# Kernel optimization log

Measured on AMD Instinct MI355X. Metric: run time of the kernel, lower is better.

Reference implementation:

```python
import jax, jax.numpy as jnp
import numpy as np

HEADS = 8


def setup_inputs() -> dict:
    key = jax.random.key(0)
    k1, k2, k3, k4, k5 = jax.random.split(key, 5)
    bt, b_sz, n, dim = 2, 4, 1024, 512
    inner6 = 3072  # inner_dim * 6 where inner_dim = heads * dim_head = 512
    return {
        "x": jax.random.normal(k1, (bt, b_sz, n, dim), dtype=jnp.float32),
        "W_qkv": jax.random.normal(k2, (dim, inner6), dtype=jnp.float32) * 0.02,
        "b_qkv": jax.random.normal(k3, (inner6,), dtype=jnp.float32) * 0.02,
        "W_out": jax.random.normal(k4, (1024, dim), dtype=jnp.float32) * 0.02,
        "b_out": jax.random.normal(k5, (dim,), dtype=jnp.float32) * 0.02,
    }


def reference(x, W_qkv, b_qkv, W_out, b_out):
    bt, b_sz, n, dim = x.shape
    # to_qkv: Linear(dim, 3072) -> reshape (bt,b,n,3,H,hd) -> transpose(2,4)
    qkv = (x @ W_qkv + b_qkv).reshape(bt, b_sz, n, 3, HEADS, -1)
    qkv = qkv.transpose(0, 1, 4, 3, 2, 5)  # (bt, b, H, 3, n, hd)
    q, k, v = qkv[:, :, :, 0], qkv[:, :, :, 1], qkv[:, :, :, 2]
    scale = (dim // HEADS) ** -0.5  # faithful: uses dim//heads, not per-head width
    attn = jax.nn.softmax(jnp.einsum("abhnd,abhmd->abhnm", q * scale, k), axis=-1)
    out = jnp.einsum("abhnm,abhmd->abhnd", attn, v)
    out = out.transpose(0, 1, 3, 2, 4).reshape(bt, b_sz, n, -1)  # (bt,b,n,H*hd)
    return out @ W_out + b_out
```

## Files before the change

kernel.cpp:

```cpp
#include <hip/hip_runtime.h>

typedef __attribute__((ext_vector_type(4))) float f32x4;
typedef __attribute__((ext_vector_type(16))) float f32x16;
typedef __attribute__((ext_vector_type(8))) __bf16 bf16x8;
typedef __attribute__((ext_vector_type(8))) unsigned short ushortx8;
typedef unsigned short u16;
typedef unsigned int u32;

#define AS1 __attribute__((address_space(1)))
#define AS3 __attribute__((address_space(3)))

__device__ __forceinline__ void gld_lds16(const void* g, void* s) {
  __builtin_amdgcn_global_load_lds((AS1 void*)g, (AS3 void*)s, 16, 0, 0);
}

__device__ __forceinline__ u16 f2bf(float f) {
  unsigned int u = __float_as_uint(f);
  unsigned int r = (u + 0x7FFFu + ((u >> 16) & 1u)) >> 16;
  return (u16)r;
}

#define QSCALE 0.1803368801111244f

__global__ void cvt_f32_bf16(const float* __restrict__ src, u16* __restrict__ dst, int n) {
  int i = (blockIdx.x * blockDim.x + threadIdx.x) * 8;
  if (i >= n) return;
  const float4 a = *(const float4*)&src[i];
  const float4 b = *(const float4*)&src[i + 4];
  ushortx8 o;
  o[0] = f2bf(a.x); o[1] = f2bf(a.y); o[2] = f2bf(a.z); o[3] = f2bf(a.w);
  o[4] = f2bf(b.x); o[5] = f2bf(b.y); o[6] = f2bf(b.z); o[7] = f2bf(b.w);
  *(ushortx8*)&dst[i] = o;
}

__global__ void scale_bias(const float* __restrict__ src, float* __restrict__ dst, int n,
                           int boundary, float s) {
  int i = blockIdx.x * blockDim.x + threadIdx.x;
  if (i < n) dst[i] = src[i] * (i < boundary ? s : 1.0f);
}

__global__ void transpose_to_bf16(const float* __restrict__ src, u16* __restrict__ dst,
                                  int R, int C, int boundary, float s) {
  __shared__ float tile[32][33];
  const int c0 = blockIdx.x * 32, r0 = blockIdx.y * 32;
  const int tx = threadIdx.x, ty = threadIdx.y;
  #pragma unroll
  for (int i = ty; i < 32; i += 8)
    tile[i][tx] = src[(size_t)(r0 + i) * C + c0 + tx];
  __syncthreads();
  #pragma unroll
  for (int i = ty; i < 32; i += 8) {
    const float sc = (c0 + i < boundary) ? s : 1.0f;
    dst[(size_t)(c0 + i) * R + r0 + tx] = f2bf(tile[tx][i] * sc);
  }
}

__global__ void transpose_v(const u16* __restrict__ qkv, u16* __restrict__ vt) {
  __shared__ u16 tile[32][34];
  const int bh = blockIdx.z, b = bh >> 3, h = bh & 7;
  const int n0 = blockIdx.y * 32, d0 = blockIdx.x * 32;
  const int tx = threadIdx.x, ty = threadIdx.y;
  const u16* src = qkv + (size_t)(b * 1024) * 3072 + 2048 + h * 128;
  #pragma unroll
  for (int i = ty; i < 32; i += 8)
    tile[i][tx] = src[(size_t)(n0 + i) * 3072 + d0 + tx];
  __syncthreads();
  u16* dst = vt + (size_t)(b * 8 + h) * 128 * 1024;
  #pragma unroll
  for (int i = ty; i < 32; i += 8)
    dst[(size_t)(d0 + i) * 1024 + n0 + tx] = tile[tx][i];
}

template <int BM, int BN, int BK, int OUT_BF16>
__global__ __launch_bounds__(256, 4) void gemm_bt(const u16* __restrict__ A,
                                                  const u16* __restrict__ Bt,
                                                  const float* __restrict__ bias,
                                                  void* __restrict__ Cv,
                                                  int M, int N, int K) {
  constexpr int RPC = 512 / BK;
  constexpr int LPR = BK / 8;
  constexpr int MASK = LPR - 1;
  constexpr int P = 64 / BK > 0 ? 64 / BK : 1;
  constexpr int CA = BM / RPC, CB = BN / RPC;
  constexpr int CAW = CA / 4, CBW = CB / 4;
  constexpr int VM = CAW + CBW;
  constexpr int FM = BM / 32, FN = BN / 32;
  constexpr int KS = BK / 32;

  __shared__ __attribute__((aligned(16))) u16 As[2][BM * BK];
  __shared__ __attribute__((aligned(16))) u16 Bs[2][BN * BK];
  const int nwg = gridDim.x * gridDim.y;
  int bid = blockIdx.y * gridDim.x + blockIdx.x;
  if ((nwg & 7) == 0) bid = (bid & 7) * (nwg >> 3) + (bid >> 3);
  const int n0 = (bid % gridDim.x) * BN, m0 = (bid / gridDim.x) * BM;
  const int tid = threadIdx.x;
  const int w = tid >> 6, l = tid & 63;
  const int wr = w >> 1, wc = w & 1;
  const int lr = l >> 4, lc = l & 15;
  f32x4 acc[FM][FN] = {};

#define GSTAGE(bi, k0)                                                          \
  do {                                                                          \
    _Pragma("unroll") for (int i = 0; i < CAW; ++i) {                           \
      const int c = w * CAW + i;                                                \
      const int row = c * RPC + l / LPR;                                        \
      const int col = ((l % LPR) ^ ((row / P) & MASK)) * 8;                     \
      gld_lds16(&A[(size_t)(m0 + row) * K + (k0) + col], &As[bi][c * 512]);     \
    }                                                                           \
    _Pragma("unroll") for (int i = 0; i < CBW; ++i) {                           \
      const int c = w * CBW + i;                                                \
      const int row = c * RPC + l / LPR;                                        \
      const int col = ((l % LPR) ^ ((row / P) & MASK)) * 8;                     \
      gld_lds16(&Bt[(size_t)(n0 + row) * K + (k0) + col], &Bs[bi][c * 512]);    \
    }                                                                           \
  } while (0)

#define GCOMP(bi)                                                                      \
  do {                                                                                 \
    _Pragma("unroll") for (int ks = 0; ks < KS; ++ks) {                                \
      bf16x8 af[FM], bfr[FN];                                                          \
      _Pragma("unroll") for (int m = 0; m < FM; ++m) {                                 \
        const int row = wr * (BM / 2) + m * 16 + lc;                                   \
        af[m] = *(const bf16x8*)&As[bi][row * BK +                                     \
                                        (((ks * 4 + lr) ^ ((row / P) & MASK)) << 3)];  \
      }                                                                                \
      _Pragma("unroll") for (int n = 0; n < FN; ++n) {                                 \
        const int row = wc * (BN / 2) + n * 16 + lc;                                   \
        bfr[n] = *(const bf16x8*)&Bs[bi][row * BK +                                    \
                                         (((ks * 4 + lr) ^ ((row / P) & MASK)) << 3)]; \
      }                                                                                \
      __builtin_amdgcn_s_setprio(1);                                                   \
      _Pragma("unroll") for (int m = 0; m < FM; ++m)                                   \
          _Pragma("unroll") for (int n = 0; n < FN; ++n)                               \
              acc[m][n] =                                                              \
          __builtin_amdgcn_mfma_f32_16x16x32_bf16(af[m], bfr[n], acc[m][n], 0, 0, 0);  \
      __builtin_amdgcn_s_setprio(0);                                                   \
    }                                                                                  \
  } while (0)

  GSTAGE(0, 0);
  int buf = 0;
  for (int k0 = BK; k0 < K; k0 += BK) {
    GSTAGE(buf ^ 1, k0);
    if constexpr (VM == 4)
      asm volatile("s_waitcnt vmcnt(4)" ::: "memory");
    else if constexpr (VM == 2)
      asm volatile("s_waitcnt vmcnt(2)" ::: "memory");
    else
      asm volatile("s_waitcnt vmcnt(8)" ::: "memory");
    __builtin_amdgcn_s_barrier();
    __builtin_amdgcn_sched_barrier(0);
    GCOMP(buf);
    __builtin_amdgcn_s_barrier();
    buf ^= 1;
  }
  asm volatile("s_waitcnt vmcnt(0)" ::: "memory");
  __builtin_amdgcn_s_barrier();
  __builtin_amdgcn_sched_barrier(0);
  GCOMP(buf);
#undef GSTAGE
#undef GCOMP

  #pragma unroll
  for (int n = 0; n < FN; ++n) {
    const int col = n0 + wc * (BN / 2) + n * 16 + lc;
    const float bv = bias[col];
    #pragma unroll
    for (int m = 0; m < FM; ++m) {
      #pragma unroll
      for (int r = 0; r < 4; ++r) {
        const int row = m0 + wr * (BM / 2) + m * 16 + lr * 4 + r;
        const float v = acc[m][n][r] + bv;
        if (OUT_BF16)
          ((u16*)Cv)[(size_t)row * N + col] = f2bf(v);
        else
          ((float*)Cv)[(size_t)row * N + col] = v;
      }
    }
  }
}

__global__ __launch_bounds__(256, 2) void attn_fwd(const u16* __restrict__ qkv,
                                                   const u16* __restrict__ vt,
                                                   u16* __restrict__ attn_out) {
  __shared__ __attribute__((aligned(16))) u16 Ks[2][64 * 128];
  __shared__ __attribute__((aligned(16))) u16 Vs[2][64 * 128];
  const int orig = blockIdx.y * 8 + blockIdx.x;
  const int swz = (orig & 7) * 64 + (orig >> 3);
  const int bh = swz >> 3, b = bh >> 3, h = bh & 7;
  const int q0 = (swz & 7) * 128;
  const int tid = threadIdx.x, w = tid >> 6, l = tid & 63;
  const int ll = l & 31, hi = l >> 5;
  const int wq0 = q0 + w * 32;
  const u16* Qb = qkv + (size_t)(b * 1024 + wq0) * 3072 + h * 128;
  const u16* Kb = qkv + (size_t)(b * 1024) * 3072 + 1024 + h * 128;
  const u16* Vb = vt + (size_t)(b * 8 + h) * 128 * 1024;

  bf16x8 bq[8];
  #pragma unroll
  for (int s = 0; s < 8; ++s)
    bq[s] = *(const bf16x8*)&Qb[(size_t)ll * 3072 + s * 16 + hi * 8];
  asm volatile("s_waitcnt vmcnt(0)" ::: "memory");

  bf16x8 ones;
  #pragma unroll
  for (int i = 0; i < 8; ++i) ones[i] = (__bf16)1.0f;

  const u16* sb[8];
  int dst0;
  if (w < 2) {
    #pragma unroll
    for (int j = 0; j < 8; ++j) {
      const int r = w * 32 + j * 4 + (l >> 4);
      const int c = l & 15;
      sb[j] = Kb + (size_t)r * 3072 + ((c ^ (r & 15)) << 3);
    }
    dst0 = w * 4096;
  } else {
    #pragma unroll
    for (int j = 0; j < 8; ++j) {
      const int r2 = (w - 2) * 32 + j * 4 + (l >> 4);
      const int c = l & 15;
      const int d = ((c >> 3) ^ ((r2 >> 3) & 1)) * 64 + (r2 >> 5) * 32 + (r2 & 31);
      const int kc = (c & 7) ^ (r2 & 7);
      sb[j] = Vb + (size_t)d * 1024 + (kc << 3);
    }
    dst0 = (w - 2) * 4096;
  }

#define STAGE(bi, tt)                                                            \
  do {                                                                           \
    if (w < 2) {                                                                 \
      _Pragma("unroll") for (int j = 0; j < 8; ++j)                              \
          gld_lds16(sb[j] + (size_t)(tt)*196608, &Ks[bi][dst0 + j * 512]);       \
    } else {                                                                     \
      _Pragma("unroll") for (int j = 0; j < 8; ++j)                              \
          gld_lds16(sb[j] + (size_t)(tt)*64, &Vs[bi][dst0 + j * 512]);           \
    }                                                                            \
  } while (0)

#define QK(Kt)                                                                     \
  do {                                                                            \
    st0 = (f32x16){};                                                             \
    st1 = (f32x16){};                                                             \
    __builtin_amdgcn_s_setprio(1);                                                \
    _Pragma("unroll") for (int s = 0; s < 8; ++s) {                               \
      const int ch = ((s * 2 + hi) ^ (ll & 15)) << 3;                             \
      const bf16x8 ak0 = *(const bf16x8*)&(Kt)[ll * 128 + ch];                    \
      const bf16x8 ak1 = *(const bf16x8*)&(Kt)[(32 + ll) * 128 + ch];             \
      st0 = __builtin_amdgcn_mfma_f32_32x32x16_bf16(ak0, bq[s], st0, 0, 0, 0);    \
      st1 = __builtin_amdgcn_mfma_f32_32x32x16_bf16(ak1, bq[s], st1, 0, 0, 0);    \
    }                                                                             \
    __builtin_amdgcn_s_setprio(0);                                                \
  } while (0)

#define SOFTMAX()                                                                  \
  do {                                                                            \
    _Pragma("unroll") for (int kb = 0; kb < 2; ++kb) {                            \
      float pe[16];                                                               \
      _Pragma("unroll") for (int r = 0; r < 16; ++r)                              \
          pe[r] = exp2f(kb ? st1[r] : st0[r]);                                    \
      _Pragma("unroll") for (int j = 0; j < 8; ++j) {                             \
        u32 d_;                                                                   \
        asm("v_cvt_pk_bf16_f32 %0, %1, %2"                                        \
            : "=v"(d_)                                                            \
            : "v"(pe[2 * j]), "v"(pe[2 * j + 1]));                                \
        mm[kb * 8 + j] = d_;                                                      \
      }                                                                           \
      asm volatile("v_permlane32_swap_b32 %0, %1"                                 \
                   : "+v"(mm[kb * 8 + 0]), "+v"(mm[kb * 8 + 2]));                 \
      asm volatile("v_permlane32_swap_b32 %0, %1"                                 \
                   : "+v"(mm[kb * 8 + 1]), "+v"(mm[kb * 8 + 3]));                 \
      asm volatile("v_permlane32_swap_b32 %0, %1"                                 \
                   : "+v"(mm[kb * 8 + 4]), "+v"(mm[kb * 8 + 6]));                 \
      asm volatile("v_permlane32_swap_b32 %0, %1"                                 \
                   : "+v"(mm[kb * 8 + 5]), "+v"(mm[kb * 8 + 7]));                 \
    }                                                                             \
  } while (0)

#define PV(Vt_)                                                                    \
  do {                                                                            \
    __builtin_amdgcn_s_setprio(1);                                                \
    _Pragma("unroll") for (int kb = 0; kb < 2; ++kb) {                            \
      _Pragma("unroll") for (int s2 = 0; s2 < 2; ++s2) {                          \
        union { u32 u[4]; bf16x8 v; } pu;                                         \
        pu.u[0] = mm[kb * 8 + s2 * 4 + 0];                                        \
        pu.u[1] = mm[kb * 8 + s2 * 4 + 1];                                        \
        pu.u[2] = mm[kb * 8 + s2 * 4 + 2];                                        \
        pu.u[3] = mm[kb * 8 + s2 * 4 + 3];                                        \
        const bf16x8 pa = pu.v;                                                   \
        acc_l = __builtin_amdgcn_mfma_f32_32x32x16_bf16(pa, ones, acc_l, 0, 0, 0);\
        _Pragma("unroll") for (int db = 0; db < 4; ++db) {                        \
          const int r2 = (db & 1) * 32 + ll;                                      \
          const int c = ((((db >> 1) ^ ((ll >> 3) & 1)) << 3) |                   \
                         ((kb * 4 + s2 * 2 + hi) ^ (ll & 7)));                    \
          const bf16x8 bv = *(const bf16x8*)&(Vt_)[r2 * 128 + c * 8];             \
          acc_o[db] =                                                             \
              __builtin_amdgcn_mfma_f32_32x32x16_bf16(pa, bv, acc_o[db], 0, 0, 0);\
        }                                                                         \
      }                                                                           \
    }                                                                             \
    __builtin_amdgcn_s_setprio(0);                                                \
  } while (0)

  f32x16 acc_o[4] = {};
  f32x16 acc_l = {};
  f32x16 st0, st1;
  u32 mm[16];

  STAGE(0, 0);
  int buf = 0;
  for (int t = 0; t < 15; ++t) {
    STAGE(buf ^ 1, t + 1);
    asm volatile("s_waitcnt vmcnt(8)" ::: "memory");
    __builtin_amdgcn_s_barrier();
    __builtin_amdgcn_sched_barrier(0);
    QK(Ks[buf]);
    SOFTMAX();
    PV(Vs[buf]);
    __builtin_amdgcn_s_barrier();
    buf ^= 1;
  }
  asm volatile("s_waitcnt vmcnt(0)" ::: "memory");
  __builtin_amdgcn_s_barrier();
  __builtin_amdgcn_sched_barrier(0);
  QK(Ks[buf]);
  SOFTMAX();
  PV(Vs[buf]);

#undef STAGE
#undef QK
#undef SOFTMAX
#undef PV

  float inv[16];
  #pragma unroll
  for (int r = 0; r < 16; ++r) inv[r] = __builtin_amdgcn_rcpf(acc_l[r]);
  u16* Ob = attn_out + (size_t)(b * 1024 + wq0) * 1024 + h * 128;
  #pragma unroll
  for (int db = 0; db < 4; ++db)
    #pragma unroll
    for (int r = 0; r < 16; ++r) {
      const int q = (r & 3) + 8 * (r >> 2) + 4 * hi;
      Ob[(size_t)q * 1024 + db * 32 + ll] = f2bf(acc_o[db][r] * inv[r]);
    }
}

extern "C" void kernel_launch(void* const* d_in, const int* in_sizes, int n_in,
                              void* d_out, int out_size, void* d_ws, size_t ws_size,
                              hipStream_t stream) {
  const float* x = (const float*)d_in[0];
  const float* Wqkv = (const float*)d_in[1];
  const float* bqkv = (const float*)d_in[2];
  const float* Wout = (const float*)d_in[3];
  const float* bout = (const float*)d_in[4];
  float* out = (float*)d_out;

  char* ws = (char*)d_ws;
  u16* xb    = (u16*)(ws);
  u16* wqkvt = (u16*)(ws + 8388608);
  u16* woutt = (u16*)(ws + 8388608 + 3145728);
  u16* qkvb  = (u16*)(ws + 12582912);
  u16* vtb   = (u16*)(ws + 62914560);
  u16* aob   = (u16*)(ws + 79691776);
  float* bq2 = (float*)aob;

  cvt_f32_bf16<<<2048, 256, 0, stream>>>(x, xb, 8192 * 512);
  scale_bias<<<12, 256, 0, stream>>>(bqkv, bq2, 3072, 1024, QSCALE);
  transpose_to_bf16<<<dim3(96, 16), dim3(32, 8), 0, stream>>>(Wqkv, wqkvt, 512, 3072, 1024, QSCALE);
  transpose_to_bf16<<<dim3(16, 32), dim3(32, 8), 0, stream>>>(Wout, woutt, 1024, 512, 0, 1.0f);

  gemm_bt<128, 128, 32, 1><<<dim3(24, 64), 256, 0, stream>>>(xb, wqkvt, bq2, qkvb,
                                                             8192, 3072, 512);

  transpose_v<<<dim3(4, 32, 64), dim3(32, 8), 0, stream>>>(qkvb, vtb);

  attn_fwd<<<dim3(8, 64), 256, 0, stream>>>(qkvb, vtb, aob);

  gemm_bt<64, 64, 32, 0><<<dim3(8, 128), 256, 0, stream>>>(aob, woutt, bout, out,
                                                           8192, 512, 1024);
}
```

Before: 130.2 us.

## Fuse prep kernels, write V transposed from QKV GEMM epilogue, retile out-proj

Merges the four preprocessing launches (x cast, bias scaling, two weight transposes) into one kernel dispatched by block index. Replaces the QKV GEMM with a new BK=64 kernel whose epilogue stages Q/K tiles through LDS for coalesced stores and writes V directly in transposed layout, removing the separate transpose_v pass. Also seeds the first QK MFMA with a zero constant instead of clearing the accumulators, and switches the output projection to 128x64 tiles with a new vmcnt case. This cuts launch overhead and one full read/write of V, at the cost of strided 8-byte V stores and larger LDS use per block.

```diff
diff --git a/kernel.cpp b/kernel.cpp
--- a/kernel.cpp
+++ b/kernel.cpp
@@ -4,6 +4,7 @@
 typedef __attribute__((ext_vector_type(16))) float f32x16;
 typedef __attribute__((ext_vector_type(8))) __bf16 bf16x8;
 typedef __attribute__((ext_vector_type(8))) unsigned short ushortx8;
+typedef __attribute__((ext_vector_type(4))) unsigned short ushortx4;
 typedef unsigned short u16;
 typedef unsigned int u32;
 
@@ -22,53 +23,52 @@
 
 #define QSCALE 0.1803368801111244f
 
-__global__ void cvt_f32_bf16(const float* __restrict__ src, u16* __restrict__ dst, int n) {
-  int i = (blockIdx.x * blockDim.x + threadIdx.x) * 8;
-  if (i >= n) return;
-  const float4 a = *(const float4*)&src[i];
-  const float4 b = *(const float4*)&src[i + 4];
-  ushortx8 o;
-  o[0] = f2bf(a.x); o[1] = f2bf(a.y); o[2] = f2bf(a.z); o[3] = f2bf(a.w);
-  o[4] = f2bf(b.x); o[5] = f2bf(b.y); o[6] = f2bf(b.z); o[7] = f2bf(b.w);
-  *(ushortx8*)&dst[i] = o;
-}
-
-__global__ void scale_bias(const float* __restrict__ src, float* __restrict__ dst, int n,
-                           int boundary, float s) {
-  int i = blockIdx.x * blockDim.x + threadIdx.x;
-  if (i < n) dst[i] = src[i] * (i < boundary ? s : 1.0f);
-}
-
-__global__ void transpose_to_bf16(const float* __restrict__ src, u16* __restrict__ dst,
-                                  int R, int C, int boundary, float s) {
+__global__ __launch_bounds__(256) void prep_fused(
+    const float* __restrict__ x, u16* __restrict__ xb,
+    const float* __restrict__ bqkv, float* __restrict__ bq2,
+    const float* __restrict__ Wqkv, u16* __restrict__ wqkvt,
+    const float* __restrict__ Wout, u16* __restrict__ woutt) {
+  const int gid = blockIdx.x, tid = threadIdx.x;
+  if (gid < 2048) {
+    const int i = (gid * 256 + tid) * 8;
+    const float4 a = *(const float4*)&x[i];
+    const float4 b = *(const float4*)&x[i + 4];
+    ushortx8 o;
+    o[0] = f2bf(a.x); o[1] = f2bf(a.y); o[2] = f2bf(a.z); o[3] = f2bf(a.w);
+    o[4] = f2bf(b.x); o[5] = f2bf(b.y); o[6] = f2bf(b.z); o[7] = f2bf(b.w);
+    *(ushortx8*)&xb[i] = o;
+    return;
+  }
   __shared__ float tile[32][33];
-  const int c0 = blockIdx.x * 32, r0 = blockIdx.y * 32;
-  const int tx = threadIdx.x, ty = threadIdx.y;
-  #pragma unroll
-  for (int i = ty; i < 32; i += 8)
-    tile[i][tx] = src[(size_t)(r0 + i) * C + c0 + tx];
-  __syncthreads();
-  #pragma unroll
-  for (int i = ty; i < 32; i += 8) {
-    const float sc = (c0 + i < boundary) ? s : 1.0f;
-    dst[(size_t)(c0 + i) * R + r0 + tx] = f2bf(tile[tx][i] * sc);
-  }
-}
-
-__global__ void transpose_v(const u16* __restrict__ qkv, u16* __restrict__ vt) {
-  __shared__ u16 tile[32][34];
-  const int bh = blockIdx.z, b = bh >> 3, h = bh & 7;
-  const int n0 = blockIdx.y * 32, d0 = blockIdx.x * 32;
-  const int tx = threadIdx.x, ty = threadIdx.y;
-  const u16* src = qkv + (size_t)(b * 1024) * 3072 + 2048 + h * 128;
-  #pragma unroll
-  for (int i = ty; i < 32; i += 8)
-    tile[i][tx] = src[(size_t)(n0 + i) * 3072 + d0 + tx];
-  __syncthreads();
-  u16* dst = vt + (size_t)(b * 8 + h) * 128 * 1024;
-  #pragma unroll
-  for (int i = ty; i < 32; i += 8)
-    dst[(size_t)(d0 + i) * 1024 + n0 + tx] = tile[tx][i];
+  const int tx = tid & 31, ty = tid >> 5;
+  if (gid < 3584) {
+    const int t = gid - 2048;
+    const int c0 = (t % 96) * 32, r0 = (t / 96) * 32;
+    #pragma unroll
+    for (int i = ty; i < 32; i += 8)
+      tile[i][tx] = Wqkv[(size_t)(r0 + i) * 3072 + c0 + tx];
+    __syncthreads();
+    #pragma unroll
+    for (int i = ty; i < 32; i += 8) {
+      const float sc = (c0 + i < 1024) ? QSCALE : 1.0f;
+      wqkvt[(size_t)(c0 + i) * 512 + r0 + tx] = f2bf(tile[tx][i] * sc);
+    }
+    return;
+  }
+  if (gid < 4096) {
+    const int t = gid - 3584;
+    const int c0 = (t % 16) * 32, r0 = (t / 16) * 32;
+    #pragma unroll
+    for (int i = ty; i < 32; i += 8)
+      tile[i][tx] = Wout[(size_t)(r0 + i) * 512 + c0 + tx];
+    __syncthreads();
+    #pragma unroll
+    for (int i = ty; i < 32; i += 8)
+      woutt[(size_t)(c0 + i) * 1024 + r0 + tx] = f2bf(tile[tx][i]);
+    return;
+  }
+  const int i = (gid - 4096) * 256 + tid;
+  if (i < 3072) bq2[i] = bqkv[i] * (i < 1024 ? QSCALE : 1.0f);
 }
 
 template <int BM, int BN, int BK, int OUT_BF16>
@@ -142,10 +142,12 @@
   int buf = 0;
   for (int k0 = BK; k0 < K; k0 += BK) {
     GSTAGE(buf ^ 1, k0);
-    if constexpr (VM == 4)
+    if constexpr (VM == 2)
+      asm volatile("s_waitcnt vmcnt(2)" ::: "memory");
+    else if constexpr (VM == 3)
+      asm volatile("s_waitcnt vmcnt(3)" ::: "memory");
+    else if constexpr (VM == 4)
       asm volatile("s_waitcnt vmcnt(4)" ::: "memory");
-    else if constexpr (VM == 2)
-      asm volatile("s_waitcnt vmcnt(2)" ::: "memory");
     else
       asm volatile("s_waitcnt vmcnt(8)" ::: "memory");
     __builtin_amdgcn_s_barrier();
@@ -175,6 +177,127 @@
           ((u16*)Cv)[(size_t)row * N + col] = f2bf(v);
         else
           ((float*)Cv)[(size_t)row * N + col] = v;
+      }
+    }
+  }
+}
+
+__global__ __launch_bounds__(256, 2) void gemm_qkv_2ph(const u16* __restrict__ A,
+                                                       const u16* __restrict__ Bt,
+                                                       const float* __restrict__ bias,
+                                                       u16* __restrict__ C,
+                                                       u16* __restrict__ vt,
+                                                       int M, int N, int K) {
+  __shared__ __attribute__((aligned(16))) u16 SMEM[32768];
+  const int nwg = gridDim.x * gridDim.y;
+  int bid = blockIdx.y * gridDim.x + blockIdx.x;
+  bid = (bid & 7) * (nwg >> 3) + (bid >> 3);
+  const int n0 = (bid % gridDim.x) * 128, m0 = (bid / gridDim.x) * 128;
+  const int tid = threadIdx.x;
+  const int w = tid >> 6, l = tid & 63;
+  const int wr = w >> 1, wc = w & 1;
+  const int lr = l >> 4, lc = l & 15;
+  f32x4 acc[4][4] = {};
+
+#define QSTAGE(bi, k0)                                                          \
+  do {                                                                          \
+    _Pragma("unroll") for (int i = 0; i < 4; ++i) {                             \
+      const int c = w * 4 + i;                                                  \
+      const int row = c * 8 + (l >> 3);                                         \
+      const int col = ((l & 7) ^ (row & 7)) * 8;                                \
+      gld_lds16(&A[(size_t)(m0 + row) * K + (k0) + col],                        \
+                &SMEM[(bi) * 8192 + c * 512]);                                  \
+    }                                                                           \
+    _Pragma("unroll") for (int i = 0; i < 4; ++i) {                             \
+      const int c = w * 4 + i;                                                  \
+      const int row = c * 8 + (l >> 3);                                         \
+      const int col = ((l & 7) ^ (row & 7)) * 8;                                \
+      gld_lds16(&Bt[(size_t)(n0 + row) * K + (k0) + col],                       \
+                &SMEM[16384 + (bi) * 8192 + c * 512]);                          \
+    }                                                                           \
+  } while (0)
+
+#define QCOMP(bi)                                                                   \
+  do {                                                                             \
+    _Pragma("unroll") for (int ks = 0; ks < 2; ++ks) {                             \
+      bf16x8 af[4], bfr[4];                                                        \
+      _Pragma("unroll") for (int m = 0; m < 4; ++m) {                              \
+        const int row = wr * 64 + m * 16 + lc;                                     \
+        af[m] = *(const bf16x8*)&SMEM[(bi) * 8192 + row * 64 +                     \
+                                      (((ks * 4 + lr) ^ (lc & 7)) << 3)];          \
+      }                                                                            \
+      _Pragma("unroll") for (int n = 0; n < 4; ++n) {                              \
+        const int row = wc * 64 + n * 16 + lc;                                     \
+        bfr[n] = *(const bf16x8*)&SMEM[16384 + (bi) * 8192 + row * 64 +            \
+                                       (((ks * 4 + lr) ^ (lc & 7)) << 3)];         \
+      }                                                                            \
+      __builtin_amdgcn_s_setprio(1);                                               \
+      _Pragma("unroll") for (int m = 0; m < 4; ++m)                                \
+          _Pragma("unroll") for (int n = 0; n < 4; ++n)                            \
+              acc[m][n] =                                                          \
+          __builtin_amdgcn_mfma_f32_16x16x32_bf16(af[m], bfr[n], acc[m][n], 0, 0, 0); \
+      __builtin_amdgcn_s_setprio(0);                                               \
+    }                                                                              \
+  } while (0)
+
+  QSTAGE(0, 0);
+  int buf = 0;
+  for (int k0 = 64; k0 < K; k0 += 64) {
+    QSTAGE(buf ^ 1, k0);
+    asm volatile("s_waitcnt vmcnt(8)" ::: "memory");
+    __builtin_amdgcn_s_barrier();
+    __builtin_amdgcn_sched_barrier(0);
+    QCOMP(buf);
+    __builtin_amdgcn_s_barrier();
+    buf ^= 1;
+  }
+  asm volatile("s_waitcnt vmcnt(0)" ::: "memory");
+  __builtin_amdgcn_s_barrier();
+  __builtin_amdgcn_sched_barrier(0);
+  QCOMP(buf);
+#undef QSTAGE
+#undef QCOMP
+
+  __builtin_amdgcn_s_barrier();
+  const int b_idx = m0 >> 10;
+  const int tok0 = m0 & 1023;
+  if (n0 < 2048) {
+    #pragma unroll
+    for (int n = 0; n < 4; ++n) {
+      const int cc = wc * 64 + n * 16 + lc;
+      const float bv = bias[n0 + cc];
+      #pragma unroll
+      for (int m = 0; m < 4; ++m)
+        #pragma unroll
+        for (int r = 0; r < 4; ++r) {
+          const int row = wr * 64 + m * 16 + lr * 4 + r;
+          SMEM[row * 128 + cc] = f2bf(acc[m][n][r] + bv);
+        }
+    }
+    __builtin_amdgcn_s_barrier();
+    #pragma unroll
+    for (int it = 0; it < 8; ++it) {
+      const int chunk = it * 256 + tid;
+      const int row = chunk >> 4, c16 = chunk & 15;
+      const bf16x8 v = *(const bf16x8*)&SMEM[row * 128 + c16 * 8];
+      *(bf16x8*)&C[(size_t)(m0 + row) * N + n0 + c16 * 8] = v;
+    }
+  } else {
+    #pragma unroll
+    for (int n = 0; n < 4; ++n) {
+      const int gc = n0 + wc * 64 + n * 16 + lc;
+      const float bv = bias[gc];
+      const int hd = gc - 2048;
+      u16* vrow = vt + ((size_t)(b_idx * 8 + (hd >> 7)) * 128 + (hd & 127)) * 1024;
+      #pragma unroll
+      for (int m = 0; m < 4; ++m) {
+        const int tok = tok0 + wr * 64 + m * 16 + lr * 4;
+        ushortx4 o;
+        o[0] = f2bf(acc[m][n][0] + bv);
+        o[1] = f2bf(acc[m][n][1] + bv);
+        o[2] = f2bf(acc[m][n][2] + bv);
+        o[3] = f2bf(acc[m][n][3] + bv);
+        *(ushortx4*)&vrow[tok] = o;
       }
     }
   }
@@ -205,6 +328,7 @@
   bf16x8 ones;
   #pragma unroll
   for (int i = 0; i < 8; ++i) ones[i] = (__bf16)1.0f;
+  const f32x16 fz = {};
 
   const u16* sb[8];
   int dst0;
@@ -241,10 +365,15 @@
 
 #define QK(Kt)                                                                     \
   do {                                                                            \
-    st0 = (f32x16){};                                                             \
-    st1 = (f32x16){};                                                             \
     __builtin_amdgcn_s_setprio(1);                                                \
-    _Pragma("unroll") for (int s = 0; s < 8; ++s) {                               \
+    {                                                                             \
+      const int ch = (hi ^ (ll & 15)) << 3;                                       \
+      const bf16x8 a0 = *(const bf16x8*)&(Kt)[ll * 128 + ch];                     \
+      const bf16x8 a1 = *(const bf16x8*)&(Kt)[(32 + ll) * 128 + ch];              \
+      st0 = __builtin_amdgcn_mfma_f32_32x32x16_bf16(a0, bq[0], fz, 0, 0, 0);      \
+      st1 = __builtin_amdgcn_mfma_f32_32x32x16_bf16(a1, bq[0], fz, 0, 0, 0);      \
+    }                                                                             \
+    _Pragma("unroll") for (int s = 1; s < 8; ++s) {                               \
       const int ch = ((s * 2 + hi) ^ (ll & 15)) << 3;                             \
       const bf16x8 ak0 = *(const bf16x8*)&(Kt)[ll * 128 + ch];                    \
       const bf16x8 ak1 = *(const bf16x8*)&(Kt)[(32 + ll) * 128 + ch];             \
@@ -365,18 +494,13 @@
   u16* aob   = (u16*)(ws + 79691776);
   float* bq2 = (float*)aob;
 
-  cvt_f32_bf16<<<2048, 256, 0, stream>>>(x, xb, 8192 * 512);
-  scale_bias<<<12, 256, 0, stream>>>(bqkv, bq2, 3072, 1024, QSCALE);
-  transpose_to_bf16<<<dim3(96, 16), dim3(32, 8), 0, stream>>>(Wqkv, wqkvt, 512, 3072, 1024, QSCALE);
-  transpose_to_bf16<<<dim3(16, 32), dim3(32, 8), 0, stream>>>(Wout, woutt, 1024, 512, 0, 1.0f);
-
-  gemm_bt<128, 128, 32, 1><<<dim3(24, 64), 256, 0, stream>>>(xb, wqkvt, bq2, qkvb,
-                                                             8192, 3072, 512);
-
-  transpose_v<<<dim3(4, 32, 64), dim3(32, 8), 0, stream>>>(qkvb, vtb);
+  prep_fused<<<4108, 256, 0, stream>>>(x, xb, bqkv, bq2, Wqkv, wqkvt, Wout, woutt);
+
+  gemm_qkv_2ph<<<dim3(24, 64), 256, 0, stream>>>(xb, wqkvt, bq2, qkvb, vtb,
+                                                 8192, 3072, 512);
 
   attn_fwd<<<dim3(8, 64), 256, 0, stream>>>(qkvb, vtb, aob);
 
-  gemm_bt<64, 64, 32, 0><<<dim3(8, 128), 256, 0, stream>>>(aob, woutt, bout, out,
+  gemm_bt<128, 64, 32, 0><<<dim3(8, 64), 256, 0, stream>>>(aob, woutt, bout, out,
                                                            8192, 512, 1024);
 }
```

Measured after the change: 117.1 us. -10.0%, faster.
